# Kernel optimization log

Hardware: AMD Instinct MI355X
Metric: run time of the kernel (lower is better)

Reference implementation:

```python
import jax, jax.numpy as jnp
import numpy as np

H = 64      # hidden width of each MLP
M_STEPS = 64   # SDE steps (m)
N_SIM = 2048   # Monte-Carlo paths (n)
D = 128        # number of options (data_size)


def _mlp4(x, W1, b1, W2, b2, W3, b3):
    # x: [n, d, 4]; weights stacked over the 4 networks on axis 0 (k)
    h = jax.nn.relu(jnp.einsum('ndf,kfh->kndh', x, W1) + b1[:, None, None, :])
    h = jax.nn.relu(jnp.einsum('kndh,khg->kndg', h, W2) + b2[:, None, None, :])
    o = jnp.einsum('kndg,kgo->kndo', h, W3) + b3[:, None, None, :]
    return jnp.tanh(o)  # [4, n, d, 1]


def setup_inputs() -> dict:
    key = jax.random.key(0)
    ks = jax.random.split(key, 12)
    S0 = jax.random.uniform(ks[0], (D,), jnp.float32, 50.0, 150.0)
    K = jax.random.uniform(ks[1], (D,), jnp.float32, 50.0, 150.0)
    T = jax.random.uniform(ks[2], (D,), jnp.float32, 0.25, 2.0)
    rf = jnp.array([0.03], jnp.float32)
    V0 = jnp.array([0.04], jnp.float32)
    rho = jnp.array([-0.5], jnp.float32)
    Z1 = jax.random.normal(ks[3], (M_STEPS, N_SIM, D), jnp.float32)
    Z2raw = jax.random.normal(ks[4], (M_STEPS, N_SIM, D), jnp.float32)
    # 4 MLPs, layers [4, H, H, 1]
    W1 = jax.random.normal(ks[5], (4, 4, H), jnp.float32) / jnp.sqrt(4.0)
    b1 = jnp.zeros((4, H), jnp.float32)
    W2 = jax.random.normal(ks[6], (4, H, H), jnp.float32) / jnp.sqrt(float(H))
    b2 = jnp.zeros((4, H), jnp.float32)
    W3 = jax.random.normal(ks[7], (4, H, 1), jnp.float32) / jnp.sqrt(float(H))
    b3 = jnp.zeros((4, 1), jnp.float32)
    return {"S0": S0, "K": K, "T": T, "rf": rf, "V0": V0, "rho": rho,
            "Z1": Z1, "Z2raw": Z2raw,
            "W1": W1, "b1": b1, "W2": W2, "b2": b2, "W3": W3, "b3": b3}


def reference(S0, K, T, rf, V0, rho, Z1, Z2raw, W1, b1, W2, b2, W3, b3):
    m, n, d = Z1.shape
    dt = (T / m)[None, :, None]          # [1, d, 1]
    sdt = jnp.sqrt(dt)
    rho_s = rho[0]
    rf_s = rf[0]
    S = jnp.broadcast_to(S0[None, :, None], (n, d, 1))
    V = jnp.broadcast_to(V0[0], (n, d, 1))

    def step(carry, xs):
        S, V = carry
        j, z1, z2r = xs                    # z1, z2r: [n, d]
        z2 = rho_s * z1 + jnp.sqrt(1.0 - rho_s ** 2) * z2r
        feat = jnp.concatenate([
            S, V,
            jnp.broadcast_to(rf_s, S.shape),
            jnp.broadcast_to(dt * j, S.shape),
        ], axis=2)                          # [n, d, 4]
        N1, N2, N3, N4 = _mlp4(feat, W1, b1, W2, b2, W3, b3)
        Vn = V * (1.0 + N3 * dt + N4 * sdt * z2[..., None])
        Sn = S * (1.0 + N1 * dt + N2 * sdt * z1[..., None])
        return (Sn, Vn), None

    js = jnp.arange(m, dtype=jnp.float32)
    (S, V), _ = jax.lax.scan(step, (S, V), (js, Z1, Z2raw))
    S = S[..., 0]                            # [n, d]
    payoff = jnp.maximum(S - K[None, :], 0.0)
    P_pred = jnp.sum(jnp.exp(-rf_s * T)[None, :] * payoff, axis=0) / n
    return P_pred
```

## Files before the change

kernel.cpp:

```cpp
#include <hip/hip_runtime.h>
#include <math.h>

#define D_OPT   128
#define N_SIM   2048
#define M_STEPS 64
#define HID     64


typedef _Float16 f16x8 __attribute__((ext_vector_type(8)));
typedef _Float16 f16x4 __attribute__((ext_vector_type(4)));
typedef _Float16 f16x2 __attribute__((ext_vector_type(2)));
typedef float    f32x4 __attribute__((ext_vector_type(4)));
typedef unsigned int u32;
typedef u32 u32x2 __attribute__((ext_vector_type(2)));
typedef u32 u32x4 __attribute__((ext_vector_type(4)));

__device__ __forceinline__ u32 pk2u(float a, float b) {
#if __has_builtin(__builtin_amdgcn_cvt_pkrtz)
    return __builtin_bit_cast(u32, __builtin_amdgcn_cvt_pkrtz(a, b));
#else
    f16x2 p; p[0] = (_Float16)a; p[1] = (_Float16)b;
    return __builtin_bit_cast(u32, p);
#endif
}

__device__ __forceinline__ u32 pk_relu_cvt(float a, float b) {
    f16x2 p = __builtin_bit_cast(f16x2, pk2u(a, b));
    const f16x2 z = { (_Float16)0.0f, (_Float16)0.0f };
#if __has_builtin(__builtin_elementwise_max)
    p = __builtin_elementwise_max(p, z);
#else
    p[0] = p[0] > z[0] ? p[0] : z[0];
    p[1] = p[1] > z[1] ? p[1] : z[1];
#endif
    return __builtin_bit_cast(u32, p);
}

__global__ __launch_bounds__(256, 4) void nsde_kernel(
    const float* __restrict__ S0p, const float* __restrict__ Kp,
    const float* __restrict__ Tp,  const float* __restrict__ rfp,
    const float* __restrict__ V0p, const float* __restrict__ rhop,
    const float* __restrict__ Z1,  const float* __restrict__ Z2r,
    const float* __restrict__ W1,  const float* __restrict__ B1,
    const float* __restrict__ W2,  const float* __restrict__ B2,
    const float* __restrict__ W3,  const float* __restrict__ B3,
    float* __restrict__ out)
{
    __shared__ float nvp[2][4][64];
    __shared__ u32x2 pkx[4][64];

    const int tid  = threadIdx.x;
    const int wave = tid >> 6;
    const int lane = tid & 63;
    const int q    = lane >> 4;
    const int mA   = lane & 15;
    const float rf = rfp[0];

    const float* w1g = W1 + wave * 256;
    const float* b1g = B1 + wave * 64;
    const float* w2g = W2 + wave * 4096;
    const float* b2g = B2 + wave * 64;
    const float* w3g = W3 + wave * 64;

    f16x4 A1[4];
    #pragma unroll
    for (int t = 0; t < 4; ++t) {
        f16x4 a = { (_Float16)0.0f, (_Float16)0.0f, (_Float16)0.0f, (_Float16)0.0f };
        if (q == 0) {
            const int h = t * 16 + mA;
            a[0] = (_Float16)w1g[0 * 64 + h];
            a[1] = (_Float16)w1g[1 * 64 + h];
            a[2] = (_Float16)w1g[3 * 64 + h];
            a[3] = (_Float16)fmaf(rf, w1g[2 * 64 + h], b1g[h]);
        }
        A1[t] = a;
    }

    f16x8 A2[4][2];
    #pragma unroll
    for (int gt = 0; gt < 4; ++gt)
        #pragma unroll
        for (int kt = 0; kt < 2; ++kt) {
            f16x8 a;
            #pragma unroll
            for (int j = 0; j < 8; ++j) {
                const int h1 = (2 * kt + (j >> 2)) * 16 + 4 * q + (j & 3);
                a[j] = (_Float16)w2g[h1 * 64 + gt * 16 + mA];
            }
            A2[gt][kt] = a;
        }

    f16x8 A3[2];
    #pragma unroll
    for (int kt = 0; kt < 2; ++kt) {
        f16x8 a;
        #pragma unroll
        for (int j = 0; j < 8; ++j) a[j] = (_Float16)0.0f;
        if (mA == 0) {
            #pragma unroll
            for (int j = 0; j < 8; ++j) {
                const int g = (2 * kt + (j >> 2)) * 16 + 4 * q + (j & 3);
                a[j] = (_Float16)w3g[g];
            }
        }
        A3[kt] = a;
    }

    f32x4 cinit2[4];
    #pragma unroll
    for (int t = 0; t < 4; ++t)
        #pragma unroll
        for (int r = 0; r < 4; ++r)
            cinit2[t][r] = b2g[t * 16 + 4 * q + r];
    const f32x4 zc = { 0.0f, 0.0f, 0.0f, 0.0f };

    const float b3n0 = B3[0], b3n1 = B3[1], b3n2 = B3[2], b3n3 = B3[3];

    const int ebase = blockIdx.x * 64;
    const int d_own = (ebase + lane) & (D_OPT - 1);
    const float dt_own  = Tp[d_own] * (1.0f / (float)M_STEPS);
    const float sdt_own = sqrtf(dt_own);

    float Sreg = S0p[d_own];
    float Vreg = V0p[0];
    {
        u32x2 pk0;
        pk0[0] = pk2u(Sreg, Vreg);
        pk0[1] = pk2u(0.0f, 1.0f);
        pkx[wave][lane] = pk0;
    }

    const float rho   = rhop[0];
    const float rho_c = sqrtf(1.0f - rho * rho);
    const size_t estep = (size_t)N_SIM * D_OPT;
    const float* z1p = Z1  + (size_t)ebase + (size_t)lane;
    const float* z2p = Z2r + (size_t)ebase + (size_t)lane;

    float z1c = *z1p;
    float z2c = *z2p;
    z1p += estep; z2p += estep;

    #pragma unroll 1
    for (int s = 0; s < M_STEPS; ++s) {
        const float z1n = *z1p;
        const float z2n = *z2p;
        const size_t adv = (s < M_STEPS - 2) ? estep : (size_t)0;
        z1p += adv; z2p += adv;

        #pragma unroll 2
        for (int mt = 0; mt < 4; ++mt) {
            const u32x2 pksv = pkx[wave][mt * 16 + mA];
            const f16x4 B1f = __builtin_bit_cast(f16x4, pksv);

            u32x4 b2u[2];
            #pragma unroll
            for (int t = 0; t < 4; ++t) {
                const f32x4 acc = __builtin_amdgcn_mfma_f32_16x16x16f16(
                                      A1[t], B1f, zc, 0, 0, 0);
                b2u[t >> 1][(t & 1) * 2 + 0] = pk_relu_cvt(acc[0], acc[1]);
                b2u[t >> 1][(t & 1) * 2 + 1] = pk_relu_cvt(acc[2], acc[3]);
            }
            const f16x8 B2f0 = __builtin_bit_cast(f16x8, b2u[0]);
            const f16x8 B2f1 = __builtin_bit_cast(f16x8, b2u[1]);

            u32x4 b3u[2];
            #pragma unroll
            for (int gt = 0; gt < 4; ++gt) {
                f32x4 acc = __builtin_amdgcn_mfma_f32_16x16x32_f16(
                                A2[gt][0], B2f0, cinit2[gt], 0, 0, 0);
                acc = __builtin_amdgcn_mfma_f32_16x16x32_f16(
                                A2[gt][1], B2f1, acc, 0, 0, 0);
                b3u[gt >> 1][(gt & 1) * 2 + 0] = pk_relu_cvt(acc[0], acc[1]);
                b3u[gt >> 1][(gt & 1) * 2 + 1] = pk_relu_cvt(acc[2], acc[3]);
            }

            f32x4 acc3 = __builtin_amdgcn_mfma_f32_16x16x32_f16(
                             A3[0], __builtin_bit_cast(f16x8, b3u[0]), zc, 0, 0, 0);
            acc3 = __builtin_amdgcn_mfma_f32_16x16x32_f16(
                             A3[1], __builtin_bit_cast(f16x8, b3u[1]), acc3, 0, 0, 0);

            if (q == 0)
                nvp[s & 1][wave][mt * 16 + mA] = acc3[0];
        }

        __builtin_amdgcn_sched_barrier(0);
        asm volatile("s_waitcnt lgkmcnt(0)\n\ts_barrier" ::: "memory");
        __builtin_amdgcn_sched_barrier(0);

        {
            const float o0 = nvp[s & 1][0][lane] + b3n0;
            const float o1 = nvp[s & 1][1][lane] + b3n1;
            const float o2 = nvp[s & 1][2][lane] + b3n2;
            const float o3 = nvp[s & 1][3][lane] + b3n3;
            const float e0 = __expf(2.0f * o0);
            const float e1 = __expf(2.0f * o1);
            const float e2 = __expf(2.0f * o2);
            const float e3 = __expf(2.0f * o3);
            const float N0 = 1.0f - 2.0f / (e0 + 1.0f);
            const float N1 = 1.0f - 2.0f / (e1 + 1.0f);
            const float N2 = 1.0f - 2.0f / (e2 + 1.0f);
            const float N3 = 1.0f - 2.0f / (e3 + 1.0f);
            const float z2 = fmaf(rho, z1c, rho_c * z2c);
            const float fS = fmaf(N1 * sdt_own, z1c, N0 * dt_own);
            const float fV = fmaf(N3 * sdt_own, z2, N2 * dt_own);
            Sreg = fmaf(Sreg, fS, Sreg);
            Vreg = fmaf(Vreg, fV, Vreg);
            u32x2 pkn;
            pkn[0] = pk2u(Sreg, Vreg);
            pkn[1] = pk2u(dt_own * (float)(s + 1), 1.0f);
            pkx[wave][lane] = pkn;
            z1c = z1n; z2c = z2n;
        }
    }

    if (wave == 0) {
        const float Td  = dt_own * (float)M_STEPS;
        const float pay = fmaxf(Sreg - Kp[d_own], 0.0f);
        atomicAdd(&out[d_own], __expf(-rf * Td) * pay * (1.0f / (float)N_SIM));
    }
}

extern "C" void kernel_launch(void* const* d_in, const int* in_sizes, int n_in,
                              void* d_out, int out_size, void* d_ws, size_t ws_size,
                              hipStream_t stream)
{
    const float* S0  = (const float*)d_in[0];
    const float* K   = (const float*)d_in[1];
    const float* T   = (const float*)d_in[2];
    const float* rf  = (const float*)d_in[3];
    const float* V0  = (const float*)d_in[4];
    const float* rho = (const float*)d_in[5];
    const float* Z1  = (const float*)d_in[6];
    const float* Z2r = (const float*)d_in[7];
    const float* W1  = (const float*)d_in[8];
    const float* B1  = (const float*)d_in[9];
    const float* W2  = (const float*)d_in[10];
    const float* B2  = (const float*)d_in[11];
    const float* W3  = (const float*)d_in[12];
    const float* B3  = (const float*)d_in[13];
    float* out = (float*)d_out;

    hipMemsetAsync(out, 0, (size_t)out_size * sizeof(float), stream);

    const int total = N_SIM * D_OPT;
    const int grid  = total / 64;
    nsde_kernel<<<grid, 256, 0, stream>>>(S0, K, T, rf, V0, rho, Z1, Z2r,
                                          W1, B1, W2, B2, W3, B3, out);
}
```

Baseline: 794.2 us.

## Process 128 paths per block to halve grid and amortize weight loads

Each block now handles 128 path/option elements instead of 64, with each thread carrying two S/V states and running eight MLP column tiles per step instead of four. The grid is halved, so the per-block setup of fp16 weight fragments and the per-step barrier are spread over twice as much work. The cost is a longer serial step per block, double the LDS buffers, and fewer blocks in flight, which may reduce the latency hiding that came from occupancy.

```diff
diff --git a/kernel.cpp b/kernel.cpp
--- a/kernel.cpp
+++ b/kernel.cpp
@@ -46,8 +46,8 @@
     const float* __restrict__ W3,  const float* __restrict__ B3,
     float* __restrict__ out)
 {
-    __shared__ float nvp[2][4][64];
-    __shared__ u32x2 pkx[4][64];
+    __shared__ float nvp[2][4][128];
+    __shared__ u32x2 pkx[4][128];
 
     const int tid  = threadIdx.x;
     const int wave = tid >> 6;
@@ -116,18 +116,25 @@
 
     const float b3n0 = B3[0], b3n1 = B3[1], b3n2 = B3[2], b3n3 = B3[3];
 
-    const int ebase = blockIdx.x * 64;
-    const int d_own = (ebase + lane) & (D_OPT - 1);
-    const float dt_own  = Tp[d_own] * (1.0f / (float)M_STEPS);
-    const float sdt_own = sqrtf(dt_own);
-
-    float Sreg = S0p[d_own];
-    float Vreg = V0p[0];
+    const int ebase = blockIdx.x * 128;
+    const int dA_ = (ebase + lane) & (D_OPT - 1);
+    const int dB_ = (ebase + 64 + lane) & (D_OPT - 1);
+    const float dtA  = Tp[dA_] * (1.0f / (float)M_STEPS);
+    const float dtB  = Tp[dB_] * (1.0f / (float)M_STEPS);
+    const float sdtA = sqrtf(dtA);
+    const float sdtB = sqrtf(dtB);
+
+    float SregA = S0p[dA_], SregB = S0p[dB_];
+    float VregA = V0p[0],   VregB = V0p[0];
     {
         u32x2 pk0;
-        pk0[0] = pk2u(Sreg, Vreg);
+        pk0[0] = pk2u(SregA, VregA);
         pk0[1] = pk2u(0.0f, 1.0f);
         pkx[wave][lane] = pk0;
+        u32x2 pk1;
+        pk1[0] = pk2u(SregB, VregB);
+        pk1[1] = pk2u(0.0f, 1.0f);
+        pkx[wave][64 + lane] = pk1;
     }
 
     const float rho   = rhop[0];
@@ -136,19 +143,19 @@
     const float* z1p = Z1  + (size_t)ebase + (size_t)lane;
     const float* z2p = Z2r + (size_t)ebase + (size_t)lane;
 
-    float z1c = *z1p;
-    float z2c = *z2p;
+    float z1cA = z1p[0], z1cB = z1p[64];
+    float z2cA = z2p[0], z2cB = z2p[64];
     z1p += estep; z2p += estep;
 
     #pragma unroll 1
     for (int s = 0; s < M_STEPS; ++s) {
-        const float z1n = *z1p;
-        const float z2n = *z2p;
+        const float z1nA = z1p[0], z1nB = z1p[64];
+        const float z2nA = z2p[0], z2nB = z2p[64];
         const size_t adv = (s < M_STEPS - 2) ? estep : (size_t)0;
         z1p += adv; z2p += adv;
 
         #pragma unroll 2
-        for (int mt = 0; mt < 4; ++mt) {
+        for (int mt = 0; mt < 8; ++mt) {
             const u32x2 pksv = pkx[wave][mt * 16 + mA];
             const f16x4 B1f = __builtin_bit_cast(f16x4, pksv);
 
@@ -200,23 +207,50 @@
             const float N1 = 1.0f - 2.0f / (e1 + 1.0f);
             const float N2 = 1.0f - 2.0f / (e2 + 1.0f);
             const float N3 = 1.0f - 2.0f / (e3 + 1.0f);
-            const float z2 = fmaf(rho, z1c, rho_c * z2c);
-            const float fS = fmaf(N1 * sdt_own, z1c, N0 * dt_own);
-            const float fV = fmaf(N3 * sdt_own, z2, N2 * dt_own);
-            Sreg = fmaf(Sreg, fS, Sreg);
-            Vreg = fmaf(Vreg, fV, Vreg);
+            const float z2 = fmaf(rho, z1cA, rho_c * z2cA);
+            const float fS = fmaf(N1 * sdtA, z1cA, N0 * dtA);
+            const float fV = fmaf(N3 * sdtA, z2, N2 * dtA);
+            SregA = fmaf(SregA, fS, SregA);
+            VregA = fmaf(VregA, fV, VregA);
             u32x2 pkn;
-            pkn[0] = pk2u(Sreg, Vreg);
-            pkn[1] = pk2u(dt_own * (float)(s + 1), 1.0f);
+            pkn[0] = pk2u(SregA, VregA);
+            pkn[1] = pk2u(dtA * (float)(s + 1), 1.0f);
             pkx[wave][lane] = pkn;
-            z1c = z1n; z2c = z2n;
+            z1cA = z1nA; z2cA = z2nA;
+        }
+        {
+            const float o0 = nvp[s & 1][0][64 + lane] + b3n0;
+            const float o1 = nvp[s & 1][1][64 + lane] + b3n1;
+            const float o2 = nvp[s & 1][2][64 + lane] + b3n2;
+            const float o3 = nvp[s & 1][3][64 + lane] + b3n3;
+            const float e0 = __expf(2.0f * o0);
+            const float e1 = __expf(2.0f * o1);
+            const float e2 = __expf(2.0f * o2);
+            const float e3 = __expf(2.0f * o3);
+            const float N0 = 1.0f - 2.0f / (e0 + 1.0f);
+            const float N1 = 1.0f - 2.0f / (e1 + 1.0f);
+            const float N2 = 1.0f - 2.0f / (e2 + 1.0f);
+            const float N3 = 1.0f - 2.0f / (e3 + 1.0f);
+            const float z2 = fmaf(rho, z1cB, rho_c * z2cB);
+            const float fS = fmaf(N1 * sdtB, z1cB, N0 * dtB);
+            const float fV = fmaf(N3 * sdtB, z2, N2 * dtB);
+            SregB = fmaf(SregB, fS, SregB);
+            VregB = fmaf(VregB, fV, VregB);
+            u32x2 pkn;
+            pkn[0] = pk2u(SregB, VregB);
+            pkn[1] = pk2u(dtB * (float)(s + 1), 1.0f);
+            pkx[wave][64 + lane] = pkn;
+            z1cB = z1nB; z2cB = z2nB;
         }
     }
 
     if (wave == 0) {
-        const float Td  = dt_own * (float)M_STEPS;
-        const float pay = fmaxf(Sreg - Kp[d_own], 0.0f);
-        atomicAdd(&out[d_own], __expf(-rf * Td) * pay * (1.0f / (float)N_SIM));
+        const float TdA = dtA * (float)M_STEPS;
+        const float pA  = fmaxf(SregA - Kp[dA_], 0.0f);
+        atomicAdd(&out[dA_], __expf(-rf * TdA) * pA * (1.0f / (float)N_SIM));
+        const float TdB = dtB * (float)M_STEPS;
+        const float pB  = fmaxf(SregB - Kp[dB_], 0.0f);
+        atomicAdd(&out[dB_], __expf(-rf * TdB) * pB * (1.0f / (float)N_SIM));
     }
 }
 
@@ -243,7 +277,7 @@
     hipMemsetAsync(out, 0, (size_t)out_size * sizeof(float), stream);
 
     const int total = N_SIM * D_OPT;
-    const int grid  = total / 64;
+    const int grid  = total / 128;
     nsde_kernel<<<grid, 256, 0, stream>>>(S0, K, T, rf, V0, rho, Z1, Z2r,
                                           W1, B1, W2, B2, W3, B3, out);
 }
```

Result: slower. 815.0 us (+2.6%).
